# Optimization experiments

Measured on AMD Instinct MI355X. Metric: run time of the kernel, lower is better.

Reference implementation:

```python
import jax, jax.numpy as jnp
import numpy as np

B, N_ENC, N_DEC = 32, 512, 512
IN_V, OUT_V = 2000, 2000
H, F, K, P = 256, 256, 5, 4  # P = |G| (indices < P are masked to 0 before embedding)
E_ENC, E_DEC = 128, 128


def setup_inputs() -> dict:
    key = jax.random.key(0)
    ks = jax.random.split(key, 16)
    s = lambda i, shape, scale=0.05: jax.random.normal(ks[i], shape, jnp.float32) * scale
    return dict(
        xs_idx=jax.random.randint(ks[0], (B, N_ENC), 0, IN_V),
        ys_idx=jax.random.randint(ks[1], (B, N_DEC), 0, OUT_V),
        gembed_W=s(2, (IN_V, F)),
        gconv_W=s(3, (K, F, F)),
        gdecode_W=s(4, (F, OUT_V)),
        enc_embed=s(5, (IN_V, E_ENC)),
        dec_embed=s(6, (OUT_V, E_DEC)),
        enc_Wih=s(7, (4 * H, E_ENC)),
        enc_Whh=s(8, (4 * H, H)),
        enc_b=jnp.zeros((4 * H,), jnp.float32),
        dec_Wih=s(9, (4 * H, E_DEC)),
        dec_Whh=s(10, (4 * H, H)),
        dec_b=jnp.zeros((4 * H,), jnp.float32),
        T=jax.random.uniform(ks[11], (H, 2 * H), jnp.float32, -0.5, 0.5),
    )


def _lstm(x, Wih, Whh, b, h0, c0):
    # x: (B, T, D); PyTorch gate order i, f, g, o
    def step(carry, xt):
        h, c = carry
        z = xt @ Wih.T + h @ Whh.T + b
        i, f, g, o = jnp.split(z, 4, axis=-1)
        c = jax.nn.sigmoid(f) * c + jax.nn.sigmoid(i) * jnp.tanh(g)
        h = jax.nn.sigmoid(o) * jnp.tanh(c)
        return (h, c), h
    (hT, cT), hs = jax.lax.scan(step, (h0, c0), jnp.swapaxes(x, 0, 1))
    return jnp.swapaxes(hs, 0, 1), hT, cT


def reference(xs_idx, ys_idx, gembed_W, gconv_W, gdecode_W, enc_embed, dec_embed,
              enc_Wih, enc_Whh, enc_b, dec_Wih, dec_Whh, dec_b, T):
    # --- G-equivariant stack: per-encoder-position distribution over output vocab ---
    e = jnp.tanh(gembed_W[xs_idx])  # (B, Ne, F)
    c = jax.lax.conv_general_dilated(e, gconv_W, (1,), 'SAME',
                                     dimension_numbers=('NWC', 'WIO', 'NWC'))
    probs = jax.nn.softmax(jnp.tanh(c) @ gdecode_W, axis=-1)  # (B, Ne, V)
    # encoder_scores[b, i, j] = probs[b, i, ys[b, j]]
    idx = jnp.broadcast_to(ys_idx[:, None, :], (probs.shape[0], probs.shape[1], ys_idx.shape[1]))
    encoder_scores = jnp.take_along_axis(probs, idx, axis=2)  # (B, Ne, Nd)

    # --- invariant LSTM encoder (indices < |G| masked to 0) ---
    xm = jnp.where(xs_idx < P, 0, xs_idx)
    x_embed = enc_embed[xm]  # (B, Ne, E)
    z = jnp.zeros((x_embed.shape[0], H), jnp.float32)
    henc, hT, cT = _lstm(x_embed, enc_Wih, enc_Whh, enc_b, z, z)
    hback, _, _ = _lstm(jnp.flip(x_embed, axis=1), enc_Wih, enc_Whh, enc_b, z, z)
    hback = jnp.flip(hback, axis=1)

    # --- decoder LSTM, initialized with encoder final state ---
    ym = jnp.where(ys_idx < P, 0, ys_idx)
    y_embed = dec_embed[ym]
    out, _, _ = _lstm(y_embed, dec_Wih, dec_Whh, dec_b, hT, cT)
    h_dec = jnp.concatenate([henc[:, -1:, :], out], axis=1)[:, :-1, :]  # (B, Nd, H)
    h_enc = jnp.concatenate([henc, hback], axis=2)  # (B, Ne, 2H)

    # --- bilinear alignment scores: eij[b, i, j] = h_dec[b, j] . (T @ h_enc[b, i]) ---
    Th = jnp.einsum('he,bie->bih', T, h_enc)           # (B, Ne, H)
    eij = jnp.einsum('bjh,bih->bij', h_dec, Th)        # (B, Ne, Nd)
    align = jax.nn.softmax(eij, axis=1)                # softmax over encoder positions

    p = jnp.sum(jnp.log(jnp.sum(encoder_scores * align, axis=1)), axis=1)  # (B,)
    return -jnp.sum(p)
```

## Files before the change

kernel.cpp:

```cpp
#include <hip/hip_runtime.h>

typedef _Float16 f16;
typedef _Float16 f16x2 __attribute__((ext_vector_type(2)));
typedef _Float16 f16x8 __attribute__((ext_vector_type(8)));
typedef float    f32x4 __attribute__((ext_vector_type(4)));
typedef int      i32x4 __attribute__((ext_vector_type(4)));
typedef unsigned int u32;
typedef unsigned short u16;

#define DEVI static __device__ __forceinline__

static constexpr int LDT = 40;
static constexpr int LDA = 264;

DEVI float sigf(float x){ return 1.f/(1.f + __expf(-x)); }
DEVI float tanh_c(float x){
  x = fminf(fmaxf(x, -15.f), 15.f);
  float e = __expf(2.f*x);
  return (e - 1.f)/(e + 1.f);
}
DEVI float sig_f(float x){ return __builtin_amdgcn_rcpf(1.f + __expf(-x)); }
DEVI float tanh_f(float x){ return 1.f - 2.f*__builtin_amdgcn_rcpf(1.f + __expf(2.f*x)); }
DEVI float wmax16(float v){
  #pragma unroll
  for (int m=1;m<16;m<<=1) v = fmaxf(v, __shfl_xor(v, m, 64));
  return v;
}
DEVI float wsum16(float v){
  #pragma unroll
  for (int m=1;m<16;m<<=1) v += __shfl_xor(v, m, 64);
  return v;
}
DEVI f16x8 frag_ld(const f16* p){ return *(const f16x8*)p; }
DEVI void stage_tileh(int t256, const f16* src, int ld, f16* dst){
  int row = t256>>2, qq = t256&3;
  *(f16x8*)(dst + row*LDT + qq*8) = *(const f16x8*)(src + (size_t)row*ld + qq*8);
}
#define ZERO4(acc) { f32x4 _z = {0.f,0.f,0.f,0.f}; acc[0]=_z; acc[1]=_z; acc[2]=_z; acc[3]=_z; }

DEVI void gemm64h(int t256, const f16* A, int lda, const f16* Bm, int ldb, int K,
                  f16* lA, f16* lB, f32x4 acc[4]){
  const int lane = t256 & 63, wv = t256 >> 6;
  const int l15 = lane & 15, kq = lane >> 4;
  for (int k0=0; k0<K; k0+=32){
    __syncthreads();
    stage_tileh(t256, A + k0, lda, lA);
    stage_tileh(t256, Bm + k0, ldb, lB);
    __syncthreads();
    f16x8 af = frag_ld(lA + (16*wv + l15)*LDT + kq*8);
    #pragma unroll
    for (int nt=0; nt<4; nt++){
      f16x8 bf = frag_ld(lB + (16*nt + l15)*LDT + kq*8);
      acc[nt] = __builtin_amdgcn_mfma_f32_16x16x32_f16(af, bf, acc[nt], 0,0,0);
    }
  }
}

__global__ void k_cvt(const float* __restrict__ s, f16* __restrict__ d, int n){
  int i = blockIdx.x*256 + threadIdx.x;
  if (i < n) d[i] = (f16)s[i];
}
__global__ void k_gconvT(const float* __restrict__ s, f16* __restrict__ d){
  int id = blockIdx.x;
  int fo = threadIdx.x;
  d[(size_t)fo*1280 + id] = (f16)s[(size_t)id*256 + fo];
}
__global__ void k_gdecT(const float* __restrict__ s, f16* __restrict__ d){
  int v = blockIdx.x, f = threadIdx.x;
  f16 val = (f16)0.f;
  if (v < 2000) val = (f16)s[(size_t)f*2000 + v];
  d[(size_t)v*256 + f] = val;
}
__global__ void k_epad(const int* __restrict__ xs, const float* __restrict__ gemb, f16* __restrict__ epad){
  int id = blockIdx.x;
  int f = threadIdx.x;
  int b = id / 516, p = id % 516;
  float v = 0.f;
  if (p >= 2 && p < 514){ int idx = xs[b*512 + p - 2]; v = tanh_c(gemb[(size_t)idx*256 + f]); }
  epad[(size_t)id*256 + f] = (f16)v;
}
__global__ void k_embx(const int* __restrict__ xs, const int* __restrict__ ys,
                       const float* __restrict__ eemb, const float* __restrict__ demb,
                       f16* __restrict__ xo, f16* __restrict__ yo){
  int id = blockIdx.x; int f = threadIdx.x;
  bool dec = id >= 32*512; int id2 = dec ? id - 32*512 : id;
  int idx = dec ? ys[id2] : xs[id2];
  if (idx < 4) idx = 0;
  const float* src = (dec ? demb : eemb) + (size_t)idx*128;
  (dec ? yo : xo)[(size_t)id2*128 + f] = (f16)src[f];
}

__global__ void k_wmax(const float* __restrict__ Whh, u32* __restrict__ ws){
  int i = (blockIdx.x*256 + threadIdx.x)*4;
  float m = 0.f;
  #pragma unroll
  for (int j=0;j<4;j++) m = fmaxf(m, fabsf(Whh[i+j]));
  #pragma unroll
  for (int d=1; d<64; d<<=1) m = fmaxf(m, __shfl_xor(m, d, 64));
  if ((threadIdx.x & 63) == 0) atomicMax(ws, __float_as_uint(m));
}
__global__ void k_wq8(const float* __restrict__ Whh, const u32* __restrict__ ws,
                      i32x4* __restrict__ Wq){
  const int bid = blockIdx.x;
  const int l = threadIdx.x;
  const int kt = bid & 3, t8 = (bid >> 2) & 7, w = bid >> 5;
  const int r15 = l & 15;
  const int u4 = r15 >> 2, g = r15 & 3;
  const int unit = w*32 + t8*4 + u4;
  const int row = g*256 + unit;
  const int k0  = kt*64 + (l >> 4)*16;
  const float scale = 127.f / __uint_as_float(ws[0]);
  int dw[4];
  #pragma unroll
  for (int d=0; d<4; d++){
    u32 acc = 0;
    #pragma unroll
    for (int j=0; j<4; j++){
      float q = __builtin_rintf(Whh[(size_t)row*256 + k0 + d*4 + j] * scale);
      int qi = (int)fminf(fmaxf(q, -127.f), 127.f);
      acc |= ((u32)qi & 0xffu) << (8*j);
    }
    dw[d] = (int)acc;
  }
  i32x4 v = { dw[0], dw[1], dw[2], dw[3] };
  Wq[(size_t)bid*64 + l] = v;
}

__global__ __launch_bounds__(256,4) void k_conv(const f16* __restrict__ epad, const f16* __restrict__ gcT, f16* __restrict__ tf){
  __shared__ f16 lA[64*LDT], lB[64*LDT];
  const int m0 = blockIdx.x*64, n0 = blockIdx.y*64;
  const int b = m0 >> 9, n = m0 & 511;
  f32x4 acc[4]; ZERO4(acc);
  gemm64h(threadIdx.x, epad + ((size_t)b*516 + n)*256, 256, gcT + (size_t)n0*1280, 1280, 1280, lA, lB, acc);
  const int lane=threadIdx.x&63, wv=threadIdx.x>>6, l15=lane&15, kq=lane>>4;
  #pragma unroll
  for (int nt=0;nt<4;nt++)
    #pragma unroll
    for (int r=0;r<4;r++)
      tf[(size_t)(m0 + 16*wv + 4*kq + r)*256 + n0 + nt*16 + l15] = (f16)tanh_c(acc[nt][r]);
}

DEVI void ku_body(int t256, int m0, int n0, const f16* X, const f16* Wih,
                  const float* bias, f16* U, f16* lA, f16* lB){
  f32x4 acc[4]; ZERO4(acc);
  gemm64h(t256, X + (size_t)m0*128, 128, Wih + (size_t)n0*128, 128, 128, lA, lB, acc);
  const int lane=t256&63, wv=t256>>6, l15=lane&15, kq=lane>>4;
  #pragma unroll
  for (int nt=0;nt<4;nt++){
    int n = n0 + nt*16 + l15;
    float bv = bias[n];
    int cnew = (n & 255)*4 + (n >> 8);
    #pragma unroll
    for (int r=0;r<4;r++)
      U[(size_t)(m0 + 16*wv + 4*kq + r)*1024 + cnew] = (f16)(acc[nt][r] + bv);
  }
}

__global__ __launch_bounds__(256,4) void k_u(const f16* __restrict__ X, const f16* __restrict__ Wih,
                                             const float* __restrict__ bias, f16* __restrict__ U){
  __shared__ f16 lA[64*LDT], lB[64*LDT];
  ku_body(threadIdx.x, blockIdx.x*64, blockIdx.y*64, X, Wih, bias, U, lA, lB);
}

DEVI void th_body(int t256, int m0, int n0, const f16* henh, const f16* Tf, f16* Th,
                  f16* lA, f16* lB){
  f32x4 acc[4]; ZERO4(acc);
  gemm64h(t256, henh + (size_t)m0*512, 512, Tf + (size_t)n0*512, 512, 512, lA, lB, acc);
  const int lane=t256&63, wv=t256>>6, l15=lane&15, kq=lane>>4;
  #pragma unroll
  for (int nt=0;nt<4;nt++)
    #pragma unroll
    for (int r=0;r<4;r++)
      Th[(size_t)(m0 + 16*wv + 4*kq + r)*256 + n0 + nt*16 + l15] = (f16)acc[nt][r];
}

DEVI void pass1_body(int tid, int mt, int ns, const f16* tf, const f16* gdT,
                     float* mxp, float* sep, f16* lA, f16* lB2, float* mxs2, float* ses2){
  const int half = tid >> 8, t256 = tid & 255;
  const int lane = tid & 63, wv = t256 >> 6, l15 = lane & 15, kq = lane >> 4;
  f16* lB = lB2 + half*(64*LDT);
  {
    const f16* A = tf + (size_t)mt*64*256;
    int row = tid >> 3, c8 = tid & 7;
    #pragma unroll
    for (int q=0;q<4;q++)
      *(f16x8*)(lA + row*LDA + c8*32 + q*8) = *(const f16x8*)(A + (size_t)row*256 + c8*32 + q*8);
  }
  if (t256 < 64){ mxs2[half*64 + t256] = -1e30f; ses2[half*64 + t256] = 0.f; }
  __syncthreads();
  for (int nci=0; nci<4; nci++){
    const int nc = half*4 + nci;
    const int nbase = ns*512 + nc*64;
    const f16* Bm = gdT + (size_t)nbase*256;
    f32x4 acc[4]; ZERO4(acc);
    for (int k0=0; k0<256; k0+=32){
      __syncthreads();
      stage_tileh(t256, Bm + k0, 256, lB);
      __syncthreads();
      f16x8 af = frag_ld(lA + (16*wv + l15)*LDA + k0 + kq*8);
      #pragma unroll
      for (int nt=0; nt<4; nt++){
        f16x8 bf = frag_ld(lB + (16*nt + l15)*LDT + kq*8);
        acc[nt] = __builtin_amdgcn_mfma_f32_16x16x32_f16(af, bf, acc[nt], 0,0,0);
      }
    }
    #pragma unroll
    for (int r=0;r<4;r++){
      float av[4]; float cm = -1e30f;
      #pragma unroll
      for (int nt=0;nt<4;nt++){
        int gcol = nbase + nt*16 + l15;
        float a = (gcol < 2000) ? acc[nt][r] : -1e30f;
        av[nt] = a; cm = fmaxf(cm, a);
      }
      cm = wmax16(cm);
      int rr = half*64 + 16*wv + 4*kq + r;
      float old = mxs2[rr];
      float nm = fmaxf(old, cm);
      float ss = 0.f;
      #pragma unroll
      for (int nt=0;nt<4;nt++) ss += __expf(av[nt] - nm);
      ss = wsum16(ss);
      if (l15 == 0){
        ses2[rr] = ses2[rr]*__expf(old - nm) + ss;
        mxs2[rr] = nm;
      }
    }
  }
  __syncthreads();
  if (tid < 64){
    float m0 = mxs2[tid], m1 = mxs2[64+tid];
    float nm = fmaxf(m0, m1);
    float se = ses2[tid]*__expf(m0-nm) + ses2[64+tid]*__expf(m1-nm);
    mxp[(size_t)ns*16384 + mt*64 + tid] = nm;
    sep[(size_t)ns*16384 + mt*64 + tid] = se;
  }
}

__global__ void k_comb1(const float* __restrict__ mxp, const float* __restrict__ sep,
                        float* __restrict__ mx, float* __restrict__ se){
  int m = blockIdx.x*256 + threadIdx.x;
  float best = -1e30f;
  #pragma unroll
  for (int k=0;k<4;k++) best = fmaxf(best, mxp[(size_t)k*16384 + m]);
  float s = 0.f;
  #pragma unroll
  for (int k=0;k<4;k++) s += sep[(size_t)k*16384 + m] * __expf(mxp[(size_t)k*16384 + m] - best);
  mx[m] = best; se[m] = s;
}

DEVI void pass2_body(int t256, int it, int jt, int b, const f16* tf, const f16* gdT,
                     const int* ys, const float* mx, const float* se, f16* scT,
                     f16* lA, f16* lB, int* jv){
  const int lane=t256&63, wv=t256>>6, l15=lane&15, kq=lane>>4;
  if (t256<64) jv[t256] = ys[b*512 + jt*64 + t256];
  const f16* A = tf + ((size_t)b*512 + it*64)*256;
  f32x4 acc[4]; ZERO4(acc);
  for (int k0=0;k0<256;k0+=32){
    __syncthreads();
    stage_tileh(t256, A + k0, 256, lA);
    { int row=t256>>2, qq=t256&3;
      *(f16x8*)(lB + row*LDT + qq*8) = *(const f16x8*)(gdT + (size_t)jv[row]*256 + k0 + qq*8); }
    __syncthreads();
    f16x8 af = frag_ld(lA + (16*wv+l15)*LDT + kq*8);
    #pragma unroll
    for (int nt=0;nt<4;nt++){
      f16x8 bf = frag_ld(lB + (16*nt+l15)*LDT + kq*8);
      acc[nt] = __builtin_amdgcn_mfma_f32_16x16x32_f16(af, bf, acc[nt], 0,0,0);
    }
  }
  float mxv[4], rsev[4];
  #pragma unroll
  for (int r=0;r<4;r++){
    int i_ = it*64 + 16*wv + 4*kq + r;
    mxv[r] = mx[b*512 + i_];
    rsev[r] = 1.f / se[b*512 + i_];
  }
  #pragma unroll
  for (int nt=0;nt<4;nt++){
    int j_ = jt*64 + nt*16 + l15;
    #pragma unroll
    for (int r=0;r<4;r++){
      int i_ = it*64 + 16*wv + 4*kq + r;
      scT[((size_t)b*512 + j_)*512 + i_] = (f16)(__expf(acc[nt][r] - mxv[r]) * rsev[r]);
    }
  }
}

__global__ __launch_bounds__(256,2) void k_final(const f16* __restrict__ hdec, const f16* __restrict__ Th,
                                                 const f16* __restrict__ scT,
                                                 float* __restrict__ pmx, float* __restrict__ pden, float* __restrict__ pnum){
  __shared__ f16 lA[64*LDA];
  __shared__ f16 lB[64*LDT];
  __shared__ float mx_s[64], den_s[64], num_s[64];
  const int is = blockIdx.x, jt = blockIdx.y, b = blockIdx.z;
  const int tid = threadIdx.x, lane=tid&63, wv=tid>>6, l15=lane&15, kq=lane>>4;
  {
    const f16* A = hdec + ((size_t)b*512 + jt*64)*256;
    int row = tid>>2, qq = tid&3;
    #pragma unroll
    for (int c=0;c<8;c++)
      *(f16x8*)(lA + row*LDA + c*32 + qq*8) = *(const f16x8*)(A + (size_t)row*256 + c*32 + qq*8);
  }
  if (tid<64){ mx_s[tid]=-1e30f; den_s[tid]=0.f; num_s[tid]=0.f; }
  __syncthreads();
  for (int ic=0; ic<4; ic++){
    const int i0 = is*256 + ic*64;
    const f16* Bm = Th + ((size_t)b*512 + i0)*256;
    f32x4 acc[4]; ZERO4(acc);
    for (int k0=0;k0<256;k0+=32){
      __syncthreads();
      stage_tileh(tid, Bm + k0, 256, lB);
      __syncthreads();
      f16x8 af = frag_ld(lA + (16*wv+l15)*LDA + k0 + kq*8);
      #pragma unroll
      for (int nt=0;nt<4;nt++){
        f16x8 bf = frag_ld(lB + (16*nt+l15)*LDT + kq*8);
        acc[nt] = __builtin_amdgcn_mfma_f32_16x16x32_f16(af, bf, acc[nt], 0,0,0);
      }
    }
    #pragma unroll
    for (int r=0;r<4;r++){
      int jl = 16*wv + 4*kq + r;
      float av[4]; float cm=-1e30f;
      #pragma unroll
      for (int nt=0;nt<4;nt++){ av[nt]=acc[nt][r]; cm=fmaxf(cm,av[nt]); }
      cm = wmax16(cm);
      float old = mx_s[jl], nm = fmaxf(old, cm);
      float ds=0.f, nsum=0.f;
      const size_t srow = ((size_t)b*512 + jt*64 + jl)*512;
      #pragma unroll
      for (int nt=0;nt<4;nt++){
        float e = __expf(av[nt]-nm);
        float sc = (float)scT[srow + i0 + nt*16 + l15];
        ds += e; nsum += sc*e;
      }
      ds = wsum16(ds); nsum = wsum16(nsum);
      if (l15==0){
        float fac = __expf(old-nm);
        den_s[jl] = den_s[jl]*fac + ds;
        num_s[jl] = num_s[jl]*fac + nsum;
        mx_s[jl] = nm;
      }
    }
  }
  __syncthreads();
  if (tid<64){
    size_t idx = (((size_t)b*512) + jt*64 + tid)*2 + is;
    pmx[idx]=mx_s[tid]; pden[idx]=den_s[tid]; pnum[idx]=num_s[tid];
  }
}

__global__ void k_comb2(const float* __restrict__ pmx, const float* __restrict__ pden,
                        const float* __restrict__ pnum, float* __restrict__ out){
  const int b = blockIdx.x, j = threadIdx.x;
  size_t base = ((size_t)b*512 + j)*2;
  float m0=pmx[base], m1=pmx[base+1];
  float m = fmaxf(m0,m1);
  float e0=__expf(m0-m), e1=__expf(m1-m);
  float den = pden[base]*e0 + pden[base+1]*e1;
  float num = pnum[base]*e0 + pnum[base+1]*e1;
  float lp = __logf(num) - __logf(den);
  __shared__ float red[512];
  red[j] = lp;
  __syncthreads();
  for (int st=256; st>0; st>>=1){ if (j<st) red[j]+=red[j+st]; __syncthreads(); }
  if (j==0) atomicAdd(out, -red[0]);
}

DEVI void lstm_core(char* smem, const f16* U, const i32x4* Wq, const u32* ws,
                    u16* hout, float* hTcT, u16* hdec0, int nsteps, int mode, int bid)
{
  f16* Ub  = (f16*)smem;
  char* h8b = smem + 16512;
  const int tid = threadIdx.x;
  const int lane = tid & 63, w = tid >> 6;
  const int l15 = lane & 15, kq = lane >> 4;
  const int s = l15 & 3, p = l15 >> 2;
  const int uA = w*32 + 8*p + kq;
  const int uB = uA + 4;

  int dir = 0, b0;
  if (mode == 0){ dir = bid >> 3; b0 = (bid & 7)*4; }
  else b0 = bid*4;

  const float zscale = __uint_as_float(ws[0]) * (1.f/(127.f*127.f));

  i32x4 aw[32];
  #pragma unroll
  for (int f=0; f<32; f++) aw[f] = Wq[(size_t)(w*32 + f)*64 + lane];

  float cA = 0.f, cB = 0.f;
  if (mode == 0){
    ((u32*)h8b)[tid] = 0u;
  } else {
    const float* hp = hTcT + (size_t)(b0+s)*512;
    float hA = hp[uA], hB = hp[uB];
    cA = hp[256 + uA]; cB = hp[256 + uB];
    h8b[((uA>>4)*4 + s)*16 + (uA&15)] = (char)(int)__builtin_rintf(hA*127.f);
    h8b[((uB>>4)*4 + s)*16 + (uB&15)] = (char)(int)__builtin_rintf(hB*127.f);
  }

  const int s_st = tid >> 7, col = (tid & 127)*8;
  {
    int tp0 = dir ? (nsteps-1) : 0;
    *(int4*)&Ub[s_st*1032 + col] = *(const int4*)(U + ((size_t)(b0+s_st)*512 + tp0)*1024 + col);
  }
  __syncthreads();

  int cur = 0;
  #pragma unroll 1
  for (int t=0; t<nsteps; ++t){
    const int tpos = dir ? (nsteps-1-t) : t;
    int tn = dir ? (nsteps-2-t >= 0 ? nsteps-2-t : 0) : (t+1 < nsteps ? t+1 : nsteps-1);
    int4 pu = *(const int4*)(U + ((size_t)(b0+s_st)*512 + tn)*1024 + col);

    const char* hc = h8b + cur*1024;
    i32x4 bf[4];
    #pragma unroll
    for (int kt=0; kt<4; kt++)
      bf[kt] = *(const i32x4*)(hc + ((kt*4 + kq)*4 + s)*16);

    i32x4 acc[8];
    #pragma unroll
    for (int t8=0; t8<8; t8++){
      i32x4 d = {0,0,0,0};
      #pragma unroll
      for (int kt=0; kt<4; kt++)
        d = __builtin_amdgcn_mfma_i32_16x16x64_i8(aw[t8*4+kt], bf[kt], d, 0,0,0);
      acc[t8] = d;
    }

    i32x4 vA, vB;
    #pragma unroll
    for (int e=0; e<4; e++){
      int x0 = (p&1) ? acc[2][e] : acc[0][e];
      int x1 = (p&1) ? acc[6][e] : acc[4][e];
      vA[e] = (p&2) ? x1 : x0;
      int y0 = (p&1) ? acc[3][e] : acc[1][e];
      int y1 = (p&1) ? acc[7][e] : acc[5][e];
      vB[e] = (p&2) ? y1 : y0;
    }

    const f16* upA = Ub + cur*4128 + s*1032 + uA*4;
    const f16* upB = Ub + cur*4128 + s*1032 + uB*4;
    float hA_, hB_;
    {
      float z0 = fmaf((float)vA[0], zscale, (float)upA[0]);
      float z1 = fmaf((float)vA[1], zscale, (float)upA[1]);
      float z2 = fmaf((float)vA[2], zscale, (float)upA[2]);
      float z3 = fmaf((float)vA[3], zscale, (float)upA[3]);
      cA = sig_f(z1)*cA + sig_f(z0)*tanh_f(z2);
      hA_ = sig_f(z3)*tanh_f(cA);
    }
    {
      float z0 = fmaf((float)vB[0], zscale, (float)upB[0]);
      float z1 = fmaf((float)vB[1], zscale, (float)upB[1]);
      float z2 = fmaf((float)vB[2], zscale, (float)upB[2]);
      float z3 = fmaf((float)vB[3], zscale, (float)upB[3]);
      cB = sig_f(z1)*cB + sig_f(z0)*tanh_f(z2);
      hB_ = sig_f(z3)*tanh_f(cB);
    }

    const int nxt = cur ^ 1;
    char* hn = h8b + nxt*1024;
    hn[((uA>>4)*4 + s)*16 + (uA&15)] = (char)(int)__builtin_rintf(hA_*127.f);
    hn[((uB>>4)*4 + s)*16 + (uB&15)] = (char)(int)__builtin_rintf(hB_*127.f);
    *(int4*)&Ub[nxt*4128 + s_st*1032 + col] = pu;

    f16 fA = (f16)hA_, fB = (f16)hB_;
    if (mode == 0){
      u16* hr = hout + ((size_t)(b0+s)*512 + tpos)*512 + dir*256;
      hr[uA] = __builtin_bit_cast(u16, fA);
      hr[uB] = __builtin_bit_cast(u16, fB);
      if (!dir && t == nsteps-1){
        hdec0[(size_t)(b0+s)*512*256 + uA] = __builtin_bit_cast(u16, fA);
        hdec0[(size_t)(b0+s)*512*256 + uB] = __builtin_bit_cast(u16, fB);
        float* hp = hTcT + (size_t)(b0+s)*512;
        hp[uA] = hA_; hp[uB] = hB_;
        hp[256+uA] = cA; hp[256+uB] = cB;
      }
    } else {
      u16* hr = hout + ((size_t)(b0+s)*512 + (t+1))*256;
      hr[uA] = __builtin_bit_cast(u16, fA);
      hr[uB] = __builtin_bit_cast(u16, fB);
    }
    __syncthreads();
    cur = nxt;
  }
}

__global__ __launch_bounds__(512,2) void k_mega_enc(
    const f16* __restrict__ Uenc, const i32x4* __restrict__ Wqe, const u32* __restrict__ wse,
    u16* __restrict__ henh, float* __restrict__ hTcT, u16* __restrict__ hdec0,
    const f16* __restrict__ tf, const f16* __restrict__ gdT,
    float* __restrict__ mxp, float* __restrict__ sep,
    const f16* __restrict__ yemb, const f16* __restrict__ Wihd,
    const float* __restrict__ db, f16* __restrict__ Udec)
{
  __shared__ __align__(16) char smem[45056];
  const int bid = blockIdx.x;
  const int tid = threadIdx.x;
  if (bid < 16){
    lstm_core(smem, Uenc, Wqe, wse, henh, hTcT, hdec0, 512, 0, bid);
  } else if (bid < 1040){
    int vb = bid - 16;
    int mt = vb >> 2;
    int ns = vb & 3;
    pass1_body(tid, mt, ns, tf, gdT, mxp, sep,
               (f16*)smem, (f16*)(smem + 33792), (float*)(smem + 44032), (float*)(smem + 44544));
  } else {
    int vb = bid - 1040;
    int half = tid >> 8, t256 = tid & 255;
    int vbm = vb >> 4, ny = vb & 15;
    int m0 = (vbm*2 + half)*64;
    int n0 = ny*64;
    char* base = smem + half*10240;
    ku_body(t256, m0, n0, yemb, Wihd, db, Udec, (f16*)base, (f16*)(base + 5120));
  }
}

__global__ __launch_bounds__(512,2) void k_mega_dec(
    const f16* __restrict__ Udec, const i32x4* __restrict__ Wqd, const u32* __restrict__ wsd,
    u16* __restrict__ hdec, float* __restrict__ hTcT,
    const f16* __restrict__ tf, const f16* __restrict__ gdT, const int* __restrict__ ys,
    const float* __restrict__ mx, const float* __restrict__ se, f16* __restrict__ scT,
    const f16* __restrict__ henh, const f16* __restrict__ Tf, f16* __restrict__ Th)
{
  __shared__ __align__(16) char smem[24576];
  const int bid = blockIdx.x;
  const int tid = threadIdx.x;
  if (bid < 8){
    lstm_core(smem, Udec, Wqd, wsd, hdec, hTcT, hdec, 511, 1, bid);
  } else if (bid < 1032){
    int vb = bid - 8;
    int half = tid >> 8, t256 = tid & 255;
    int b = vb >> 5, rem = vb & 31;
    int jt = rem >> 2, it = (rem & 3)*2 + half;
    char* base = smem + half*10496;
    pass2_body(t256, it, jt, b, tf, gdT, ys, mx, se, scT,
               (f16*)base, (f16*)(base + 5120), (int*)(base + 10240));
  } else {
    int vb = bid - 1032;
    int half = tid >> 8, t256 = tid & 255;
    int m0 = ((vb >> 2)*2 + half)*64;
    int n0 = (vb & 3)*64;
    char* base = smem + half*10240;
    th_body(t256, m0, n0, henh, Tf, Th, (f16*)base, (f16*)(base + 5120));
  }
}

extern "C" void kernel_launch(void* const* d_in, const int* in_sizes, int n_in,
                              void* d_out, int out_size, void* d_ws, size_t ws_size,
                              hipStream_t stream)
{
  (void)in_sizes; (void)n_in; (void)out_size;
  const int*   xs    = (const int*)d_in[0];
  const int*   ys    = (const int*)d_in[1];
  const float* gemb  = (const float*)d_in[2];
  const float* gconv = (const float*)d_in[3];
  const float* gdec  = (const float*)d_in[4];
  const float* eemb  = (const float*)d_in[5];
  const float* demb  = (const float*)d_in[6];
  const float* eWih  = (const float*)d_in[7];
  const float* eWhh  = (const float*)d_in[8];
  const float* eb    = (const float*)d_in[9];
  const float* dWih  = (const float*)d_in[10];
  const float* dWhh  = (const float*)d_in[11];
  const float* db    = (const float*)d_in[12];
  const float* Tm    = (const float*)d_in[13];

  char* wsb = (char*)d_ws;
  size_t off = 0;
  auto take = [&](size_t bytes)->char*{ char* p = wsb + off; off += (bytes + 255) & ~(size_t)255; return p; };
  f16* epad  = (f16*)take((size_t)32*516*256*2);
  f16* tf    = (f16*)take((size_t)32*512*256*2);
  f16* xemb  = (f16*)take((size_t)32*512*128*2);
  f16* yemb  = (f16*)take((size_t)32*512*128*2);
  f16* Uenc  = (f16*)take((size_t)32*512*1024*2);
  f16* Udec  = (f16*)take((size_t)32*512*1024*2);
  f16* henh  = (f16*)take((size_t)32*512*512*2);
  f16* hdec  = (f16*)take((size_t)32*512*256*2);
  f16* Th    = (f16*)take((size_t)32*512*256*2);
  f16* scT   = (f16*)take((size_t)32*512*512*2);
  float* mx  = (float*)take((size_t)16384*4);
  float* se  = (float*)take((size_t)16384*4);
  float* mxp = (float*)take((size_t)4*16384*4);
  float* sep = (float*)take((size_t)4*16384*4);
  float* pmx = (float*)take((size_t)32*512*2*4);
  float* pden= (float*)take((size_t)32*512*2*4);
  float* pnum= (float*)take((size_t)32*512*2*4);
  float* hTcT= (float*)take((size_t)32*512*4);
  f16* Wihe  = (f16*)take((size_t)1024*128*2);
  f16* Wihd  = (f16*)take((size_t)1024*128*2);
  f16* Tf    = (f16*)take((size_t)256*512*2);
  f16* gcT   = (f16*)take((size_t)256*1280*2);
  f16* gdT   = (f16*)take((size_t)2048*256*2);
  i32x4* Wq8e = (i32x4*)take((size_t)256*64*16);
  i32x4* Wq8d = (i32x4*)take((size_t)256*64*16);
  u32* wsc   = (u32*)take(8);
  if (off > ws_size) return;

  hipMemsetAsync(d_out, 0, sizeof(float), stream);
  hipMemsetAsync(wsc, 0, 8, stream);

  k_cvt<<<dim3(512),  256, 0, stream>>>(eWih, Wihe, 1024*128);
  k_cvt<<<dim3(512),  256, 0, stream>>>(dWih, Wihd, 1024*128);
  k_cvt<<<dim3(512),  256, 0, stream>>>(Tm,   Tf,   256*512);
  k_gconvT<<<dim3(1280), 256, 0, stream>>>(gconv, gcT);
  k_gdecT <<<dim3(2048), 256, 0, stream>>>(gdec, gdT);
  k_wmax<<<dim3(256), 256, 0, stream>>>(eWhh, wsc + 0);
  k_wmax<<<dim3(256), 256, 0, stream>>>(dWhh, wsc + 1);
  k_wq8<<<dim3(256), 64, 0, stream>>>(eWhh, wsc + 0, Wq8e);
  k_wq8<<<dim3(256), 64, 0, stream>>>(dWhh, wsc + 1, Wq8d);
  k_epad<<<dim3(32*516), 256, 0, stream>>>(xs, gemb, epad);
  k_embx<<<dim3(2*32*512), 128, 0, stream>>>(xs, ys, eemb, demb, xemb, yemb);

  k_conv<<<dim3(256,4), 256, 0, stream>>>(epad, gcT, tf);
  k_u<<<dim3(256,16), 256, 0, stream>>>(xemb, Wihe, eb, Uenc);

  k_mega_enc<<<dim3(3088), 512, 0, stream>>>(Uenc, Wq8e, wsc + 0, (u16*)henh, hTcT, (u16*)hdec,
                                             tf, gdT, mxp, sep, yemb, Wihd, db, Udec);
  k_comb1<<<dim3(64), 256, 0, stream>>>(mxp, sep, mx, se);

  k_mega_dec<<<dim3(1544), 512, 0, stream>>>(Udec, Wq8d, wsc + 1, (u16*)hdec, hTcT,
                                             tf, gdT, ys, mx, se, scT, henh, Tf, Th);

  k_final<<<dim3(2,8,32), 256, 0, stream>>>(hdec, Th, scT, pmx, pden, pnum);
  k_comb2<<<dim3(32), 512, 0, stream>>>(pmx, pden, pnum, (float*)d_out);
}
```

Before: 1.182 ms.

## Merge prep kernels, fuse final combine, and defer LSTM hidden-state stores

Folds eleven small preprocessing launches into three grid-partitioned kernels (prep1/prep2/prep3). It also removes the two-way split in the final alignment kernel so each block covers all encoder positions and reduces directly into the output, which eliminates the k_comb2 launch and its partial buffers. Inside the LSTM recurrence, the per-step f16 hidden-state global stores are deferred by one step and issued at the top of the next iteration, so they overlap with the following step's work instead of sitting before the barrier. The risks are lower parallelism in the final kernel (256 blocks instead of 512) and extra live registers in the recurrent loop.

```diff
diff --git a/kernel.cpp b/kernel.cpp
--- a/kernel.cpp
+++ b/kernel.cpp
@@ -13,7 +13,6 @@
 static constexpr int LDT = 40;
 static constexpr int LDA = 264;
 
-DEVI float sigf(float x){ return 1.f/(1.f + __expf(-x)); }
 DEVI float tanh_c(float x){
   x = fminf(fmaxf(x, -15.f), 15.f);
   float e = __expf(2.f*x);
@@ -56,54 +55,41 @@
   }
 }
 
-__global__ void k_cvt(const float* __restrict__ s, f16* __restrict__ d, int n){
-  int i = blockIdx.x*256 + threadIdx.x;
-  if (i < n) d[i] = (f16)s[i];
-}
-__global__ void k_gconvT(const float* __restrict__ s, f16* __restrict__ d){
-  int id = blockIdx.x;
-  int fo = threadIdx.x;
-  d[(size_t)fo*1280 + id] = (f16)s[(size_t)id*256 + fo];
-}
-__global__ void k_gdecT(const float* __restrict__ s, f16* __restrict__ d){
-  int v = blockIdx.x, f = threadIdx.x;
-  f16 val = (f16)0.f;
-  if (v < 2000) val = (f16)s[(size_t)f*2000 + v];
-  d[(size_t)v*256 + f] = val;
-}
-__global__ void k_epad(const int* __restrict__ xs, const float* __restrict__ gemb, f16* __restrict__ epad){
-  int id = blockIdx.x;
-  int f = threadIdx.x;
-  int b = id / 516, p = id % 516;
-  float v = 0.f;
-  if (p >= 2 && p < 514){ int idx = xs[b*512 + p - 2]; v = tanh_c(gemb[(size_t)idx*256 + f]); }
-  epad[(size_t)id*256 + f] = (f16)v;
-}
-__global__ void k_embx(const int* __restrict__ xs, const int* __restrict__ ys,
-                       const float* __restrict__ eemb, const float* __restrict__ demb,
-                       f16* __restrict__ xo, f16* __restrict__ yo){
-  int id = blockIdx.x; int f = threadIdx.x;
-  bool dec = id >= 32*512; int id2 = dec ? id - 32*512 : id;
-  int idx = dec ? ys[id2] : xs[id2];
-  if (idx < 4) idx = 0;
-  const float* src = (dec ? demb : eemb) + (size_t)idx*128;
-  (dec ? yo : xo)[(size_t)id2*128 + f] = (f16)src[f];
-}
-
-__global__ void k_wmax(const float* __restrict__ Whh, u32* __restrict__ ws){
-  int i = (blockIdx.x*256 + threadIdx.x)*4;
-  float m = 0.f;
-  #pragma unroll
-  for (int j=0;j<4;j++) m = fmaxf(m, fabsf(Whh[i+j]));
-  #pragma unroll
-  for (int d=1; d<64; d<<=1) m = fmaxf(m, __shfl_xor(m, d, 64));
-  if ((threadIdx.x & 63) == 0) atomicMax(ws, __float_as_uint(m));
-}
-__global__ void k_wq8(const float* __restrict__ Whh, const u32* __restrict__ ws,
-                      i32x4* __restrict__ Wq){
-  const int bid = blockIdx.x;
-  const int l = threadIdx.x;
-  const int kt = bid & 3, t8 = (bid >> 2) & 7, w = bid >> 5;
+__global__ __launch_bounds__(256) void k_prep1(
+    const float* __restrict__ eWih, const float* __restrict__ dWih, const float* __restrict__ Tm,
+    const float* __restrict__ gconv, const float* __restrict__ gdec,
+    const float* __restrict__ eWhh, const float* __restrict__ dWhh,
+    f16* __restrict__ Wihe, f16* __restrict__ Wihd, f16* __restrict__ Tf,
+    f16* __restrict__ gcT, f16* __restrict__ gdT, u32* __restrict__ wsc)
+{
+  const int bid = blockIdx.x, tid = threadIdx.x;
+  if (bid < 512){ int i = bid*256 + tid; Wihe[i] = (f16)eWih[i]; }
+  else if (bid < 1024){ int i = (bid-512)*256 + tid; Wihd[i] = (f16)dWih[i]; }
+  else if (bid < 1536){ int i = (bid-1024)*256 + tid; Tf[i] = (f16)Tm[i]; }
+  else if (bid < 2816){
+    int id = bid - 1536;
+    gcT[(size_t)tid*1280 + id] = (f16)gconv[(size_t)id*256 + tid];
+  } else if (bid < 4864){
+    int v = bid - 2816;
+    f16 val = (f16)0.f;
+    if (v < 2000) val = (f16)gdec[(size_t)tid*2000 + v];
+    gdT[(size_t)v*256 + tid] = val;
+  } else {
+    const float* W = (bid < 5120) ? eWhh : dWhh;
+    u32* ws = wsc + ((bid < 5120) ? 0 : 1);
+    int sb = (bid < 5120) ? (bid - 4864) : (bid - 5120);
+    int i = (sb*256 + tid)*4;
+    float m = 0.f;
+    #pragma unroll
+    for (int j=0;j<4;j++) m = fmaxf(m, fabsf(W[i+j]));
+    #pragma unroll
+    for (int d=1; d<64; d<<=1) m = fmaxf(m, __shfl_xor(m, d, 64));
+    if ((tid & 63) == 0) atomicMax(ws, __float_as_uint(m));
+  }
+}
+
+DEVI void wq8_body(const float* Whh, const u32* ws, i32x4* Wq, int frag, int l){
+  const int kt = frag & 3, t8 = (frag >> 2) & 7, w = frag >> 5;
   const int r15 = l & 15;
   const int u4 = r15 >> 2, g = r15 & 3;
   const int unit = w*32 + t8*4 + u4;
@@ -123,16 +109,45 @@
     dw[d] = (int)acc;
   }
   i32x4 v = { dw[0], dw[1], dw[2], dw[3] };
-  Wq[(size_t)bid*64 + l] = v;
-}
-
-__global__ __launch_bounds__(256,4) void k_conv(const f16* __restrict__ epad, const f16* __restrict__ gcT, f16* __restrict__ tf){
-  __shared__ f16 lA[64*LDT], lB[64*LDT];
-  const int m0 = blockIdx.x*64, n0 = blockIdx.y*64;
+  Wq[(size_t)frag*64 + l] = v;
+}
+
+__global__ __launch_bounds__(256) void k_prep2(
+    const float* __restrict__ eWhh, const float* __restrict__ dWhh, const u32* __restrict__ wsc,
+    i32x4* __restrict__ Wq8e, i32x4* __restrict__ Wq8d,
+    const int* __restrict__ xs, const int* __restrict__ ys,
+    const float* __restrict__ gemb, const float* __restrict__ eemb, const float* __restrict__ demb,
+    f16* __restrict__ epad, f16* __restrict__ xemb, f16* __restrict__ yemb)
+{
+  const int bid = blockIdx.x, tid = threadIdx.x;
+  if (bid < 64){
+    wq8_body(eWhh, wsc + 0, Wq8e, bid*4 + (tid >> 6), tid & 63);
+  } else if (bid < 128){
+    wq8_body(dWhh, wsc + 1, Wq8d, (bid-64)*4 + (tid >> 6), tid & 63);
+  } else if (bid < 128 + 16512){
+    int id = bid - 128;
+    int b = id / 516, p = id % 516;
+    float v = 0.f;
+    if (p >= 2 && p < 514){ int idx = xs[b*512 + p - 2]; v = tanh_c(gemb[(size_t)idx*256 + tid]); }
+    epad[(size_t)id*256 + tid] = (f16)v;
+  } else {
+    int vb = bid - (128 + 16512);
+    int id = vb*2 + (tid >> 7);
+    int f = tid & 127;
+    bool dec = id >= 32*512; int id2 = dec ? id - 32*512 : id;
+    int idx = dec ? ys[id2] : xs[id2];
+    if (idx < 4) idx = 0;
+    const float* src = (dec ? demb : eemb) + (size_t)idx*128;
+    (dec ? yemb : xemb)[(size_t)id2*128 + f] = (f16)src[f];
+  }
+}
+
+DEVI void conv_body(int t256, int m0, int n0, const f16* epad, const f16* gcT, f16* tf,
+                    f16* lA, f16* lB){
   const int b = m0 >> 9, n = m0 & 511;
   f32x4 acc[4]; ZERO4(acc);
-  gemm64h(threadIdx.x, epad + ((size_t)b*516 + n)*256, 256, gcT + (size_t)n0*1280, 1280, 1280, lA, lB, acc);
-  const int lane=threadIdx.x&63, wv=threadIdx.x>>6, l15=lane&15, kq=lane>>4;
+  gemm64h(t256, epad + ((size_t)b*516 + n)*256, 256, gcT + (size_t)n0*1280, 1280, 1280, lA, lB, acc);
+  const int lane=t256&63, wv=t256>>6, l15=lane&15, kq=lane>>4;
   #pragma unroll
   for (int nt=0;nt<4;nt++)
     #pragma unroll
@@ -156,10 +171,19 @@
   }
 }
 
-__global__ __launch_bounds__(256,4) void k_u(const f16* __restrict__ X, const f16* __restrict__ Wih,
-                                             const float* __restrict__ bias, f16* __restrict__ U){
+__global__ __launch_bounds__(256,4) void k_prep3(
+    const f16* __restrict__ epad, const f16* __restrict__ gcT, f16* __restrict__ tf,
+    const f16* __restrict__ xemb, const f16* __restrict__ Wihe,
+    const float* __restrict__ eb, f16* __restrict__ Uenc)
+{
   __shared__ f16 lA[64*LDT], lB[64*LDT];
-  ku_body(threadIdx.x, blockIdx.x*64, blockIdx.y*64, X, Wih, bias, U, lA, lB);
+  const int bid = blockIdx.x;
+  if (bid < 1024){
+    conv_body(threadIdx.x, (bid >> 2)*64, (bid & 3)*64, epad, gcT, tf, lA, lB);
+  } else {
+    int vb = bid - 1024;
+    ku_body(threadIdx.x, (vb >> 4)*64, (vb & 15)*64, xemb, Wihe, eb, Uenc, lA, lB);
+  }
 }
 
 DEVI void th_body(int t256, int m0, int n0, const f16* henh, const f16* Tf, f16* Th,
@@ -287,13 +311,12 @@
   }
 }
 
-__global__ __launch_bounds__(256,2) void k_final(const f16* __restrict__ hdec, const f16* __restrict__ Th,
-                                                 const f16* __restrict__ scT,
-                                                 float* __restrict__ pmx, float* __restrict__ pden, float* __restrict__ pnum){
+__global__ __launch_bounds__(256,2) void k_final2(const f16* __restrict__ hdec, const f16* __restrict__ Th,
+                                                  const f16* __restrict__ scT, float* __restrict__ out){
   __shared__ f16 lA[64*LDA];
   __shared__ f16 lB[64*LDT];
   __shared__ float mx_s[64], den_s[64], num_s[64];
-  const int is = blockIdx.x, jt = blockIdx.y, b = blockIdx.z;
+  const int jt = blockIdx.x, b = blockIdx.y;
   const int tid = threadIdx.x, lane=tid&63, wv=tid>>6, l15=lane&15, kq=lane>>4;
   {
     const f16* A = hdec + ((size_t)b*512 + jt*64)*256;
@@ -304,8 +327,8 @@
   }
   if (tid<64){ mx_s[tid]=-1e30f; den_s[tid]=0.f; num_s[tid]=0.f; }
   __syncthreads();
-  for (int ic=0; ic<4; ic++){
-    const int i0 = is*256 + ic*64;
+  for (int ic=0; ic<8; ic++){
+    const int i0 = ic*64;
     const f16* Bm = Th + ((size_t)b*512 + i0)*256;
     f32x4 acc[4]; ZERO4(acc);
     for (int k0=0;k0<256;k0+=32){
@@ -345,27 +368,12 @@
     }
   }
   __syncthreads();
-  if (tid<64){
-    size_t idx = (((size_t)b*512) + jt*64 + tid)*2 + is;
-    pmx[idx]=mx_s[tid]; pden[idx]=den_s[tid]; pnum[idx]=num_s[tid];
-  }
-}
-
-__global__ void k_comb2(const float* __restrict__ pmx, const float* __restrict__ pden,
-                        const float* __restrict__ pnum, float* __restrict__ out){
-  const int b = blockIdx.x, j = threadIdx.x;
-  size_t base = ((size_t)b*512 + j)*2;
-  float m0=pmx[base], m1=pmx[base+1];
-  float m = fmaxf(m0,m1);
-  float e0=__expf(m0-m), e1=__expf(m1-m);
-  float den = pden[base]*e0 + pden[base+1]*e1;
-  float num = pnum[base]*e0 + pnum[base+1]*e1;
-  float lp = __logf(num) - __logf(den);
-  __shared__ float red[512];
-  red[j] = lp;
-  __syncthreads();
-  for (int st=256; st>0; st>>=1){ if (j<st) red[j]+=red[j+st]; __syncthreads(); }
-  if (j==0) atomicAdd(out, -red[0]);
+  if (tid < 64){
+    float lp = __logf(num_s[tid]) - __logf(den_s[tid]);
+    #pragma unroll
+    for (int m=1;m<64;m<<=1) lp += __shfl_xor(lp, m, 64);
+    if (tid == 0) atomicAdd(out, -lp);
+  }
 }
 
 DEVI void lstm_core(char* smem, const f16* U, const i32x4* Wq, const u32* ws,
@@ -409,8 +417,15 @@
   __syncthreads();
 
   int cur = 0;
+  u32 pk_pend = 0;
+  u16* pr_pend = hout;
+  float hA_l = 0.f, hB_l = 0.f;
   #pragma unroll 1
   for (int t=0; t<nsteps; ++t){
+    if (t > 0){
+      pr_pend[0] = (u16)(pk_pend & 0xffffu);
+      pr_pend[4] = (u16)(pk_pend >> 16);
+    }
     const int tpos = dir ? (nsteps-1-t) : t;
     int tn = dir ? (nsteps-2-t >= 0 ? nsteps-2-t : 0) : (t+1 < nsteps ? t+1 : nsteps-1);
     int4 pu = *(const int4*)(U + ((size_t)(b0+s_st)*512 + tn)*1024 + col);
@@ -444,14 +459,13 @@
 
     const f16* upA = Ub + cur*4128 + s*1032 + uA*4;
     const f16* upB = Ub + cur*4128 + s*1032 + uB*4;
-    float hA_, hB_;
     {
       float z0 = fmaf((float)vA[0], zscale, (float)upA[0]);
       float z1 = fmaf((float)vA[1], zscale, (float)upA[1]);
       float z2 = fmaf((float)vA[2], zscale, (float)upA[2]);
       float z3 = fmaf((float)vA[3], zscale, (float)upA[3]);
       cA = sig_f(z1)*cA + sig_f(z0)*tanh_f(z2);
-      hA_ = sig_f(z3)*tanh_f(cA);
+      hA_l = sig_f(z3)*tanh_f(cA);
     }
     {
       float z0 = fmaf((float)vB[0], zscale, (float)upB[0]);
@@ -459,34 +473,33 @@
       float z2 = fmaf((float)vB[2], zscale, (float)upB[2]);
       float z3 = fmaf((float)vB[3], zscale, (float)upB[3]);
       cB = sig_f(z1)*cB + sig_f(z0)*tanh_f(z2);
-      hB_ = sig_f(z3)*tanh_f(cB);
+      hB_l = sig_f(z3)*tanh_f(cB);
     }
 
     const int nxt = cur ^ 1;
     char* hn = h8b + nxt*1024;
-    hn[((uA>>4)*4 + s)*16 + (uA&15)] = (char)(int)__builtin_rintf(hA_*127.f);
-    hn[((uB>>4)*4 + s)*16 + (uB&15)] = (char)(int)__builtin_rintf(hB_*127.f);
+    hn[((uA>>4)*4 + s)*16 + (uA&15)] = (char)(int)__builtin_rintf(hA_l*127.f);
+    hn[((uB>>4)*4 + s)*16 + (uB&15)] = (char)(int)__builtin_rintf(hB_l*127.f);
     *(int4*)&Ub[nxt*4128 + s_st*1032 + col] = pu;
 
-    f16 fA = (f16)hA_, fB = (f16)hB_;
-    if (mode == 0){
-      u16* hr = hout + ((size_t)(b0+s)*512 + tpos)*512 + dir*256;
-      hr[uA] = __builtin_bit_cast(u16, fA);
-      hr[uB] = __builtin_bit_cast(u16, fB);
-      if (!dir && t == nsteps-1){
-        hdec0[(size_t)(b0+s)*512*256 + uA] = __builtin_bit_cast(u16, fA);
-        hdec0[(size_t)(b0+s)*512*256 + uB] = __builtin_bit_cast(u16, fB);
-        float* hp = hTcT + (size_t)(b0+s)*512;
-        hp[uA] = hA_; hp[uB] = hB_;
-        hp[256+uA] = cA; hp[256+uB] = cB;
-      }
-    } else {
-      u16* hr = hout + ((size_t)(b0+s)*512 + (t+1))*256;
-      hr[uA] = __builtin_bit_cast(u16, fA);
-      hr[uB] = __builtin_bit_cast(u16, fB);
-    }
+    f16 fA = (f16)hA_l, fB = (f16)hB_l;
+    pk_pend = (u32)__builtin_bit_cast(u16, fA) | ((u32)__builtin_bit_cast(u16, fB) << 16);
+    if (mode == 0)
+      pr_pend = hout + ((size_t)(b0+s)*512 + tpos)*512 + dir*256 + uA;
+    else
+      pr_pend = hout + ((size_t)(b0+s)*512 + (t+1))*256 + uA;
+
     __syncthreads();
     cur = nxt;
+  }
+  pr_pend[0] = (u16)(pk_pend & 0xffffu);
+  pr_pend[4] = (u16)(pk_pend >> 16);
+  if (mode == 0 && !dir){
+    hdec0[(size_t)(b0+s)*512*256 + uA] = (u16)(pk_pend & 0xffffu);
+    hdec0[(size_t)(b0+s)*512*256 + uB] = (u16)(pk_pend >> 16);
+    float* hp = hTcT + (size_t)(b0+s)*512;
+    hp[uA] = hA_l; hp[uB] = hB_l;
+    hp[256+uA] = cA; hp[256+uB] = cB;
   }
 }
 
@@ -587,9 +600,6 @@
   float* se  = (float*)take((size_t)16384*4);
   float* mxp = (float*)take((size_t)4*16384*4);
   float* sep = (float*)take((size_t)4*16384*4);
-  float* pmx = (float*)take((size_t)32*512*2*4);
-  float* pden= (float*)take((size_t)32*512*2*4);
-  float* pnum= (float*)take((size_t)32*512*2*4);
   float* hTcT= (float*)take((size_t)32*512*4);
   f16* Wihe  = (f16*)take((size_t)1024*128*2);
   f16* Wihd  = (f16*)take((size_t)1024*128*2);
@@ -604,20 +614,12 @@
   hipMemsetAsync(d_out, 0, sizeof(float), stream);
   hipMemsetAsync(wsc, 0, 8, stream);
 
-  k_cvt<<<dim3(512),  256, 0, stream>>>(eWih, Wihe, 1024*128);
-  k_cvt<<<dim3(512),  256, 0, stream>>>(dWih, Wihd, 1024*128);
-  k_cvt<<<dim3(512),  256, 0, stream>>>(Tm,   Tf,   256*512);
-  k_gconvT<<<dim3(1280), 256, 0, stream>>>(gconv, gcT);
-  k_gdecT <<<dim3(2048), 256, 0, stream>>>(gdec, gdT);
-  k_wmax<<<dim3(256), 256, 0, stream>>>(eWhh, wsc + 0);
-  k_wmax<<<dim3(256), 256, 0, stream>>>(dWhh, wsc + 1);
-  k_wq8<<<dim3(256), 64, 0, stream>>>(eWhh, wsc + 0, Wq8e);
-  k_wq8<<<dim3(256), 64, 0, stream>>>(dWhh, wsc + 1, Wq8d);
-  k_epad<<<dim3(32*516), 256, 0, stream>>>(xs, gemb, epad);
-  k_embx<<<dim3(2*32*512), 128, 0, stream>>>(xs, ys, eemb, demb, xemb, yemb);
-
-  k_conv<<<dim3(256,4), 256, 0, stream>>>(epad, gcT, tf);
-  k_u<<<dim3(256,16), 256, 0, stream>>>(xemb, Wihe, eb, Uenc);
+  k_prep1<<<dim3(5376), 256, 0, stream>>>(eWih, dWih, Tm, gconv, gdec, eWhh, dWhh,
+                                          Wihe, Wihd, Tf, gcT, gdT, wsc);
+  k_prep2<<<dim3(128 + 16512 + 16384), 256, 0, stream>>>(eWhh, dWhh, wsc, Wq8e, Wq8d,
+                                                         xs, ys, gemb, eemb, demb,
+                                                         epad, xemb, yemb);
+  k_prep3<<<dim3(5120), 256, 0, stream>>>(epad, gcT, tf, xemb, Wihe, eb, Uenc);
 
   k_mega_enc<<<dim3(3088), 512, 0, stream>>>(Uenc, Wq8e, wsc + 0, (u16*)henh, hTcT, (u16*)hdec,
                                              tf, gdT, mxp, sep, yemb, Wihd, db, Udec);
@@ -626,6 +628,5 @@
   k_mega_dec<<<dim3(1544), 512, 0, stream>>>(Udec, Wq8d, wsc + 1, (u16*)hdec, hTcT,
                                              tf, gdT, ys, mx, se, scT, henh, Tf, Th);
 
-  k_final<<<dim3(2,8,32), 256, 0, stream>>>(hdec, Th, scT, pmx, pden, pnum);
-  k_comb2<<<dim3(32), 512, 0, stream>>>(pmx, pden, pnum, (float*)d_out);
-}
+  k_final2<<<dim3(8,32), 256, 0, stream>>>(hdec, Th, scT, (float*)d_out);
+}
```

Measured after the change: 1.202 ms. Within noise of the previous version (+1.8%).
